# Optimization experiments

Hardware: AMD Instinct MI355X
Metric: run time of the kernel (lower is better)

## Reference

```python
import jax, jax.numpy as jnp
import numpy as np

IN_CH, OUT_CH, KS = 64, 128, 3
GRID, DEG = 8, 3
STRIDE, PAD = 1, 1
SIZE = IN_CH * KS * KS            # 576
NCOEF = GRID + DEG                # 11
GRID_RANGE = (-1.0, 1.0)


def _xavier_uniform(key, shape):
    fan_out, fan_in = shape
    a = float(np.sqrt(6.0 / (fan_in + fan_out)))
    return jax.random.uniform(key, shape, minval=-a, maxval=a, dtype=jnp.float32)


def setup_inputs() -> dict:
    key = jax.random.key(0)
    k1, k2, k3 = jax.random.split(key, 3)
    x = jax.random.normal(k1, (8, IN_CH, 32, 32), dtype=jnp.float32)
    # non-trainable knot grid, one row per unfolded feature
    knots = jnp.tile(jnp.linspace(GRID_RANGE[0], GRID_RANGE[1], GRID + 1, dtype=jnp.float32)[None, :], (SIZE, 1))
    coeff = 0.1 * jax.random.normal(k2, (OUT_CH, SIZE, NCOEF), dtype=jnp.float32)
    base_weights = _xavier_uniform(k3, (OUT_CH, SIZE))
    spline_weights = jnp.ones((OUT_CH, SIZE), dtype=jnp.float32)
    return {"x": x, "knots": knots, "coeff": coeff,
            "base_weights": base_weights, "spline_weights": spline_weights}


def bspline_basis(x, grid, k):
    # x: (S, P) evaluation points; grid: (S, G+1) knots. Returns (S, G+k, P).
    h = (grid[:, -1:] - grid[:, :1]) / (grid.shape[1] - 1)
    left = grid[:, :1] - h * jnp.arange(k, 0, -1, dtype=x.dtype)
    right = grid[:, -1:] + h * jnp.arange(1, k + 1, dtype=x.dtype)
    g = jnp.concatenate([left, grid, right], axis=1)  # (S, G+1+2k)
    xe = x[:, None, :]
    B = ((xe >= g[:, :-1, None]) & (xe < g[:, 1:, None])).astype(x.dtype)
    for d in range(1, k + 1):  # de Boor recursion over fixed degree
        B = ((xe - g[:, :-(d + 1), None]) / (g[:, d:-1, None] - g[:, :-(d + 1), None]) * B[:, :-1]
             + (g[:, d + 1:, None] - xe) / (g[:, d + 1:, None] - g[:, 1:-d, None]) * B[:, 1:])
    return B


def _unfold(x):
    # torch F.unfold with channel-major (c, kh, kw) feature ordering
    N, C, H, W = x.shape
    xp = jnp.pad(x, ((0, 0), (0, 0), (PAD, PAD), (PAD, PAD)))
    Hp = (H + 2 * PAD - KS) // STRIDE + 1
    Wp = (W + 2 * PAD - KS) // STRIDE + 1
    patches = jnp.stack([xp[:, :, i:i + STRIDE * Hp:STRIDE, j:j + STRIDE * Wp:STRIDE]
                         for i in range(KS) for j in range(KS)], axis=2)  # (N, C, KS*KS, Hp, Wp)
    L = Hp * Wp
    u = patches.reshape(N, SIZE, L)              # (N, size, L)
    u = jnp.transpose(u, (1, 0, 2)).reshape(SIZE, N * L)  # (size, N*L), col = n*L + l
    return u, Hp, Wp


def reference(x, knots, coeff, base_weights, spline_weights):
    N = x.shape[0]
    u, Hp, Wp = _unfold(x)                                   # (size, P)
    base = base_weights @ jax.nn.silu(u)                     # (Cout, P)
    B = bspline_basis(u, knots, DEG)                         # (size, ncoef, P)
    eff = spline_weights[:, :, None] * coeff                 # (Cout, size, ncoef)
    spl = jnp.einsum('csj,sjp->cp', eff, B)                  # (Cout, P)
    out = (base + spl).reshape(OUT_CH, N, Hp, Wp)
    return jnp.transpose(out, (1, 0, 2, 3))                  # (N, Cout, Hp, Wp)
```

## Files before the change

kernel.cpp:

```cpp
#include <hip/hip_runtime.h>


typedef __attribute__((ext_vector_type(8))) short bf16x8;
typedef __attribute__((ext_vector_type(4))) float f32x4;
typedef __attribute__((ext_vector_type(16))) float f32x16;
typedef __attribute__((ext_vector_type(4))) unsigned short u16x4;

#define WSWZ_BYTES 1769472
#define PHI_OFF    WSWZ_BYTES
#define PHI_BYTES  14205696
#define PART_OFF   (PHI_OFF + PHI_BYTES)

__device__ __forceinline__ short f2bf(float f) {
    union { float f; unsigned u; } c; c.f = f;
    unsigned r = c.u + 0x7fffu + ((c.u >> 16) & 1u);
    return (short)(r >> 16);
}
__device__ __forceinline__ float bf2f(unsigned short u) {
    union { unsigned u; float f; } c; c.u = ((unsigned)u) << 16;
    return c.f;
}

__global__ void kan_prep(const float* __restrict__ coeff,
                         const float* __restrict__ basew,
                         const float* __restrict__ splw,
                         const float* __restrict__ x,
                         short* __restrict__ Wswz,
                         short* __restrict__ Phi) {
    __shared__ float coeffL[6336];
    __shared__ float basewL[576];
    __shared__ float splwL[576];
    __shared__ unsigned short xs[64 * 32];
    const int t = threadIdx.x;

    if (blockIdx.x < 272) {
        const int rowid = blockIdx.x;
        const int n     = rowid / 34;
        const int ypad  = rowid - n * 34;
        const int y     = ypad - 1;
        const bool yvalid = (y >= 0 && y < 32);

        if (yvalid) {
#pragma unroll
            for (int it = 0; it < 2; ++it) {
                int cg = t + it * 256;
                int ci = cg >> 3, q = cg & 7;
                f32x4 v = *(const f32x4*)(x + (((n * 64 + ci) * 32 + y) * 32 + q * 4));
                u16x4 p;
                p.x = (unsigned short)f2bf(v.x); p.y = (unsigned short)f2bf(v.y);
                p.z = (unsigned short)f2bf(v.z); p.w = (unsigned short)f2bf(v.w);
                *(u16x4*)&xs[ci * 32 + q * 4] = p;
            }
        }
        __syncthreads();

        const size_t rowbase = (size_t)rowid * 12 * 2176;
        for (int it = t; it < 272; it += 256) {
            int xp = it >> 3, cch = it & 7, c0 = cch << 3;
            bool interior = yvalid && (xp >= 1 && xp <= 32);
            int px = xp - 1;
            int pxc = px < 0 ? 0 : (px > 31 ? 31 : px);
            bf16x8 packs[12];
#pragma unroll
            for (int j = 0; j < 8; ++j) {
                float v = interior ? bf2f(xs[(c0 + j) * 32 + pxc]) : 0.f;
                float tt = 4.f * v + 7.f;
                int   i0 = -100;
                float b0 = 0.f, b1 = 0.f, b2 = 0.f, b3 = 0.f;
                if (tt >= 0.f && tt < 14.f) {
                    i0 = (int)tt;
                    float fr  = tt - (float)i0;
                    float omf = 1.f - fr;
                    float fr2 = fr * fr, fr3 = fr2 * fr;
                    b0 = omf * omf * omf * (1.f / 6.f);
                    b1 = (3.f * fr3 - 6.f * fr2 + 4.f) * (1.f / 6.f);
                    b2 = (-3.f * fr3 + 3.f * fr2 + 3.f * fr + 1.f) * (1.f / 6.f);
                    b3 = fr3 * (1.f / 6.f);
                }
                float silu = v * __builtin_amdgcn_rcpf(1.f + __expf(-v));
                packs[0][j] = f2bf(silu);
#pragma unroll
                for (int f = 1; f < 12; ++f) {
                    int jj = f - 1;
                    float val = 0.f;
                    val = (jj == i0 - 3) ? b0 : val;
                    val = (jj == i0 - 2) ? b1 : val;
                    val = (jj == i0 - 1) ? b2 : val;
                    val = (jj == i0    ) ? b3 : val;
                    packs[f][j] = f2bf(val);
                }
            }
            int swz = (cch ^ (xp & 7)) << 3;
#pragma unroll
            for (int f = 0; f < 12; ++f)
                *(bf16x8*)&Phi[rowbase + (size_t)f * 2176 + xp * 64 + swz] = packs[f];
        }
    } else {
        const int co = blockIdx.x - 272;
        const float* crow = coeff + co * 6336;
        for (int i = t; i < 6336; i += 256) coeffL[i] = crow[i];
        for (int i = t; i < 576; i += 256) {
            basewL[i] = basew[co * 576 + i];
            splwL[i]  = splw[co * 576 + i];
        }
        __syncthreads();
        const int cb = co >> 5, lm = co & 31;
        for (int c = t; c < 864; c += 256) {
            int kk16 = c >> 1, kh = c & 1;
            int f  = kk16 / 36;
            int rm = kk16 - f * 36;
            int tap = rm >> 2, q = rm & 3;
            bf16x8 pack;
#pragma unroll
            for (int j = 0; j < 8; ++j) {
                int ci = q * 16 + kh * 8 + j;
                int s  = ci * 9 + tap;
                float v = (f == 0) ? basewL[s] : splwL[s] * coeffL[s * 11 + (f - 1)];
                pack[j] = f2bf(v);
            }
            *(bf16x8*)(Wswz + (size_t)((kk16 * 4 + cb) * 64 + kh * 32 + lm) * 8) = pack;
        }
    }
}

__global__ __launch_bounds__(256, 4)
void kan_gemm(const short* __restrict__ Phi,
              const short* __restrict__ Wswz,
              float* __restrict__ part) {
    __shared__ short Bs[2 * 8704];

    const int t  = threadIdx.x;
    const int w  = t >> 6;
    const int l  = t & 63;
    const int ln = l & 31;
    const int kh = l >> 5;

    const int fg    = blockIdx.x >> 7;
    const int ptile = blockIdx.x & 127;
    const int n     = ptile >> 4;
    const int y0    = (ptile & 15) << 1;

    const char* phiB = (const char*)Phi;
    const int planeBase = (n * 34 + y0) * 12 + fg * 2;
#pragma unroll
    for (int k = 0; k < 9; ++k) {
        int i = t + k * 256;
        if (i < 2176) {
            int pl  = i / 1088;
            int r2  = i - pl * 1088;
            int row = r2 / 272;
            int m   = r2 - row * 272;
            const char* s = phiB + (size_t)(planeBase + row * 12 + pl) * 4352 + m * 16;
            auto gsrc = (const __attribute__((address_space(1))) unsigned int*)s;
            auto ldst = (__attribute__((address_space(3))) unsigned int*)((char*)&Bs[0] + i * 16);
            __builtin_amdgcn_global_load_lds(gsrc, ldst, 16, 0, 0);
        }
    }
    __syncthreads();

    f32x16 acc[2];
#pragma unroll
    for (int pb = 0; pb < 2; ++pb)
#pragma unroll
        for (int r = 0; r < 16; ++r)
            acc[pb][r] = 0.f;

    const short* Abase = Wswz + (size_t)w * 512 + (size_t)l * 8;
#pragma unroll 1
    for (int p = 0; p < 2; ++p) {
        const short* B0 = Bs + p * 8704;
        const int kbase = (fg * 2 + p) * 36;
#pragma unroll
        for (int q = 0; q < 4; ++q) {
#pragma unroll
            for (int dx = 0; dx < 3; ++dx) {
                bf16x8 a0 = *(const bf16x8*)(Abase + (size_t)(kbase + (0 * 3 + dx) * 4 + q) * 2048);
                bf16x8 a1 = *(const bf16x8*)(Abase + (size_t)(kbase + (1 * 3 + dx) * 4 + q) * 2048);
                bf16x8 a2 = *(const bf16x8*)(Abase + (size_t)(kbase + (2 * 3 + dx) * 4 + q) * 2048);
                const int c   = q * 2 + kh;
                const int key = (ln + dx) & 7;
                bf16x8 b0, b1, b2, b3;
                {
                    int pix0 = 0 * 34 + ln + dx;
                    int pix1 = 1 * 34 + ln + dx;
                    int pix2 = 2 * 34 + ln + dx;
                    int pix3 = 3 * 34 + ln + dx;
                    int slot = (c ^ key) << 3;
                    b0 = *(const bf16x8*)&B0[pix0 * 64 + slot];
                    b1 = *(const bf16x8*)&B0[pix1 * 64 + slot];
                    b2 = *(const bf16x8*)&B0[pix2 * 64 + slot];
                    b3 = *(const bf16x8*)&B0[pix3 * 64 + slot];
                }
                acc[0] = __builtin_amdgcn_mfma_f32_32x32x16_bf16(a0, b0, acc[0], 0, 0, 0);
                acc[1] = __builtin_amdgcn_mfma_f32_32x32x16_bf16(a0, b1, acc[1], 0, 0, 0);
                acc[0] = __builtin_amdgcn_mfma_f32_32x32x16_bf16(a1, b1, acc[0], 0, 0, 0);
                acc[1] = __builtin_amdgcn_mfma_f32_32x32x16_bf16(a1, b2, acc[1], 0, 0, 0);
                acc[0] = __builtin_amdgcn_mfma_f32_32x32x16_bf16(a2, b2, acc[0], 0, 0, 0);
                acc[1] = __builtin_amdgcn_mfma_f32_32x32x16_bf16(a2, b3, acc[1], 0, 0, 0);
            }
        }
    }

    float* dst = part + (size_t)fg * 1048576;
#pragma unroll
    for (int pb = 0; pb < 2; ++pb) {
        int y = y0 + pb;
#pragma unroll
        for (int r = 0; r < 16; ++r) {
            int row = (r & 3) + 8 * (r >> 2) + 4 * kh;
            int co  = w * 32 + row;
            dst[((size_t)(n * 128 + co) * 32 + y) * 32 + ln] = acc[pb][r];
        }
    }
}

__global__ void kan_reduce(const float* __restrict__ part,
                           float* __restrict__ out) {
    const int r = blockIdx.x;
    const int p = r & 127;
    const int i = r >> 7;
    const int n  = p >> 4;
    const int yp = p & 15;
    const int c  = i * 256 + threadIdx.x;
    const int co = c >> 4;
    const int rem = c & 15;
    const int yy = rem >> 3, xq = rem & 7;
    const size_t idx = ((size_t)(n * 128 + co) * 32 + yp * 2 + yy) * 8 + xq;
    f32x4 a = ((const f32x4*)part)[idx];
#pragma unroll
    for (int s = 1; s < 6; ++s)
        a += ((const f32x4*)(part + (size_t)s * 1048576))[idx];
    ((f32x4*)out)[idx] = a;
}

extern "C" void kernel_launch(void* const* d_in, const int* in_sizes, int n_in,
                              void* d_out, int out_size, void* d_ws, size_t ws_size,
                              hipStream_t stream) {
    const float* x     = (const float*)d_in[0];
    const float* coeff = (const float*)d_in[2];
    const float* basew = (const float*)d_in[3];
    const float* splw  = (const float*)d_in[4];
    float* out = (float*)d_out;

    short* Wswz = (short*)d_ws;
    short* Phi  = (short*)((char*)d_ws + PHI_OFF);
    float* part = (float*)((char*)d_ws + PART_OFF);

    kan_prep<<<400, 256, 0, stream>>>(coeff, basew, splw, x, Wswz, Phi);
    kan_gemm<<<768, 256, 0, stream>>>(Phi, Wswz, part);
    kan_reduce<<<1024, 256, 0, stream>>>(part, out);
}
```

Measured before the change: 107.1 us.

## Fuse prep, GEMM and reduce into one cooperative kernel with grid syncs

Merges the three kernel launches into a single cooperative kernel of 768 blocks that uses grid.sync() between the prep, GEMM and reduce phases, sharing one static LDS buffer. The goal is to remove two kernel launch gaps and their tail effects. If the cooperative launch fails, it falls back to the original three launches. The cost is that the fused kernel uses the largest LDS footprint across all phases, which may reduce occupancy, and grid-wide barriers can be slow on a device with many CUs.

```diff
diff --git a/kernel.cpp b/kernel.cpp
--- a/kernel.cpp
+++ b/kernel.cpp
@@ -1,4 +1,7 @@
 #include <hip/hip_runtime.h>
+#include <hip/hip_cooperative_groups.h>
+
+namespace cg = cooperative_groups;
 
 
 typedef __attribute__((ext_vector_type(8))) short bf16x8;
@@ -21,124 +24,116 @@
     return c.f;
 }
 
-__global__ void kan_prep(const float* __restrict__ coeff,
-                         const float* __restrict__ basew,
-                         const float* __restrict__ splw,
-                         const float* __restrict__ x,
-                         short* __restrict__ Wswz,
-                         short* __restrict__ Phi) {
-    __shared__ float coeffL[6336];
-    __shared__ float basewL[576];
-    __shared__ float splwL[576];
-    __shared__ unsigned short xs[64 * 32];
-    const int t = threadIdx.x;
-
-    if (blockIdx.x < 272) {
-        const int rowid = blockIdx.x;
-        const int n     = rowid / 34;
-        const int ypad  = rowid - n * 34;
-        const int y     = ypad - 1;
-        const bool yvalid = (y >= 0 && y < 32);
-
-        if (yvalid) {
-#pragma unroll
-            for (int it = 0; it < 2; ++it) {
-                int cg = t + it * 256;
-                int ci = cg >> 3, q = cg & 7;
-                f32x4 v = *(const f32x4*)(x + (((n * 64 + ci) * 32 + y) * 32 + q * 4));
-                u16x4 p;
-                p.x = (unsigned short)f2bf(v.x); p.y = (unsigned short)f2bf(v.y);
-                p.z = (unsigned short)f2bf(v.z); p.w = (unsigned short)f2bf(v.w);
-                *(u16x4*)&xs[ci * 32 + q * 4] = p;
+
+__device__ __forceinline__ void prep_phi_body(int rowid, int t,
+                                              const float* __restrict__ x,
+                                              short* __restrict__ Phi,
+                                              unsigned short* xs ) {
+    const int n     = rowid / 34;
+    const int ypad  = rowid - n * 34;
+    const int y     = ypad - 1;
+    const bool yvalid = (y >= 0 && y < 32);
+
+    if (yvalid) {
+#pragma unroll
+        for (int it = 0; it < 2; ++it) {
+            int cg = t + it * 256;
+            int ci = cg >> 3, q = cg & 7;
+            f32x4 v = *(const f32x4*)(x + (((n * 64 + ci) * 32 + y) * 32 + q * 4));
+            u16x4 p;
+            p.x = (unsigned short)f2bf(v.x); p.y = (unsigned short)f2bf(v.y);
+            p.z = (unsigned short)f2bf(v.z); p.w = (unsigned short)f2bf(v.w);
+            *(u16x4*)&xs[ci * 32 + q * 4] = p;
+        }
+    }
+    __syncthreads();
+
+    const size_t rowbase = (size_t)rowid * 12 * 2176;
+    for (int it = t; it < 272; it += 256) {
+        int xp = it >> 3, cch = it & 7, c0 = cch << 3;
+        bool interior = yvalid && (xp >= 1 && xp <= 32);
+        int px = xp - 1;
+        int pxc = px < 0 ? 0 : (px > 31 ? 31 : px);
+        bf16x8 packs[12];
+#pragma unroll
+        for (int j = 0; j < 8; ++j) {
+            float v = interior ? bf2f(xs[(c0 + j) * 32 + pxc]) : 0.f;
+            float tt = 4.f * v + 7.f;
+            int   i0 = -100;
+            float b0 = 0.f, b1 = 0.f, b2 = 0.f, b3 = 0.f;
+            if (tt >= 0.f && tt < 14.f) {
+                i0 = (int)tt;
+                float fr  = tt - (float)i0;
+                float omf = 1.f - fr;
+                float fr2 = fr * fr, fr3 = fr2 * fr;
+                b0 = omf * omf * omf * (1.f / 6.f);
+                b1 = (3.f * fr3 - 6.f * fr2 + 4.f) * (1.f / 6.f);
+                b2 = (-3.f * fr3 + 3.f * fr2 + 3.f * fr + 1.f) * (1.f / 6.f);
+                b3 = fr3 * (1.f / 6.f);
             }
-        }
-        __syncthreads();
-
-        const size_t rowbase = (size_t)rowid * 12 * 2176;
-        for (int it = t; it < 272; it += 256) {
-            int xp = it >> 3, cch = it & 7, c0 = cch << 3;
-            bool interior = yvalid && (xp >= 1 && xp <= 32);
-            int px = xp - 1;
-            int pxc = px < 0 ? 0 : (px > 31 ? 31 : px);
-            bf16x8 packs[12];
-#pragma unroll
-            for (int j = 0; j < 8; ++j) {
-                float v = interior ? bf2f(xs[(c0 + j) * 32 + pxc]) : 0.f;
-                float tt = 4.f * v + 7.f;
-                int   i0 = -100;
-                float b0 = 0.f, b1 = 0.f, b2 = 0.f, b3 = 0.f;
-                if (tt >= 0.f && tt < 14.f) {
-                    i0 = (int)tt;
-                    float fr  = tt - (float)i0;
-                    float omf = 1.f - fr;
-                    float fr2 = fr * fr, fr3 = fr2 * fr;
-                    b0 = omf * omf * omf * (1.f / 6.f);
-                    b1 = (3.f * fr3 - 6.f * fr2 + 4.f) * (1.f / 6.f);
-                    b2 = (-3.f * fr3 + 3.f * fr2 + 3.f * fr + 1.f) * (1.f / 6.f);
-                    b3 = fr3 * (1.f / 6.f);
-                }
-                float silu = v * __builtin_amdgcn_rcpf(1.f + __expf(-v));
-                packs[0][j] = f2bf(silu);
-#pragma unroll
-                for (int f = 1; f < 12; ++f) {
-                    int jj = f - 1;
-                    float val = 0.f;
-                    val = (jj == i0 - 3) ? b0 : val;
-                    val = (jj == i0 - 2) ? b1 : val;
-                    val = (jj == i0 - 1) ? b2 : val;
-                    val = (jj == i0    ) ? b3 : val;
-                    packs[f][j] = f2bf(val);
-                }
+            float silu = v * __builtin_amdgcn_rcpf(1.f + __expf(-v));
+            packs[0][j] = f2bf(silu);
+#pragma unroll
+            for (int f = 1; f < 12; ++f) {
+                int jj = f - 1;
+                float val = 0.f;
+                val = (jj == i0 - 3) ? b0 : val;
+                val = (jj == i0 - 2) ? b1 : val;
+                val = (jj == i0 - 1) ? b2 : val;
+                val = (jj == i0    ) ? b3 : val;
+                packs[f][j] = f2bf(val);
             }
-            int swz = (cch ^ (xp & 7)) << 3;
-#pragma unroll
-            for (int f = 0; f < 12; ++f)
-                *(bf16x8*)&Phi[rowbase + (size_t)f * 2176 + xp * 64 + swz] = packs[f];
-        }
-    } else {
-        const int co = blockIdx.x - 272;
-        const float* crow = coeff + co * 6336;
-        for (int i = t; i < 6336; i += 256) coeffL[i] = crow[i];
-        for (int i = t; i < 576; i += 256) {
-            basewL[i] = basew[co * 576 + i];
-            splwL[i]  = splw[co * 576 + i];
-        }
-        __syncthreads();
-        const int cb = co >> 5, lm = co & 31;
-        for (int c = t; c < 864; c += 256) {
-            int kk16 = c >> 1, kh = c & 1;
-            int f  = kk16 / 36;
-            int rm = kk16 - f * 36;
-            int tap = rm >> 2, q = rm & 3;
-            bf16x8 pack;
-#pragma unroll
-            for (int j = 0; j < 8; ++j) {
-                int ci = q * 16 + kh * 8 + j;
-                int s  = ci * 9 + tap;
-                float v = (f == 0) ? basewL[s] : splwL[s] * coeffL[s * 11 + (f - 1)];
-                pack[j] = f2bf(v);
-            }
-            *(bf16x8*)(Wswz + (size_t)((kk16 * 4 + cb) * 64 + kh * 32 + lm) * 8) = pack;
-        }
-    }
-}
-
-__global__ __launch_bounds__(256, 4)
-void kan_gemm(const short* __restrict__ Phi,
-              const short* __restrict__ Wswz,
-              float* __restrict__ part) {
-    __shared__ short Bs[2 * 8704];
-
-    const int t  = threadIdx.x;
+        }
+        int swz = (cch ^ (xp & 7)) << 3;
+#pragma unroll
+        for (int f = 0; f < 12; ++f)
+            *(bf16x8*)&Phi[rowbase + (size_t)f * 2176 + xp * 64 + swz] = packs[f];
+    }
+}
+
+__device__ __forceinline__ void prep_w_body(int co, int t,
+                                            const float* __restrict__ coeff,
+                                            const float* __restrict__ basew,
+                                            const float* __restrict__ splw,
+                                            short* __restrict__ Wswz,
+                                            float* coeffL, float* basewL,
+                                            float* splwL) {
+    const float* crow = coeff + co * 6336;
+    for (int i = t; i < 6336; i += 256) coeffL[i] = crow[i];
+    for (int i = t; i < 576; i += 256) {
+        basewL[i] = basew[co * 576 + i];
+        splwL[i]  = splw[co * 576 + i];
+    }
+    __syncthreads();
+    const int cb = co >> 5, lm = co & 31;
+    for (int c = t; c < 864; c += 256) {
+        int kk16 = c >> 1, kh = c & 1;
+        int f  = kk16 / 36;
+        int rm = kk16 - f * 36;
+        int tap = rm >> 2, q = rm & 3;
+        bf16x8 pack;
+#pragma unroll
+        for (int j = 0; j < 8; ++j) {
+            int ci = q * 16 + kh * 8 + j;
+            int s  = ci * 9 + tap;
+            float v = (f == 0) ? basewL[s] : splwL[s] * coeffL[s * 11 + (f - 1)];
+            pack[j] = f2bf(v);
+        }
+        *(bf16x8*)(Wswz + (size_t)((kk16 * 4 + cb) * 64 + kh * 32 + lm) * 8) = pack;
+    }
+}
+
+__device__ __forceinline__ void gemm_body(int fg, int ptile, int t,
+                                          const short* __restrict__ Phi,
+                                          const short* __restrict__ Wswz,
+                                          float* __restrict__ part,
+                                          short* Bs ) {
     const int w  = t >> 6;
     const int l  = t & 63;
     const int ln = l & 31;
     const int kh = l >> 5;
-
-    const int fg    = blockIdx.x >> 7;
-    const int ptile = blockIdx.x & 127;
-    const int n     = ptile >> 4;
-    const int y0    = (ptile & 15) << 1;
+    const int n  = ptile >> 4;
+    const int y0 = (ptile & 15) << 1;
 
     const char* phiB = (const char*)Phi;
     const int planeBase = (n * 34 + y0) * 12 + fg * 2;
@@ -151,9 +146,10 @@
             int row = r2 / 272;
             int m   = r2 - row * 272;
             const char* s = phiB + (size_t)(planeBase + row * 12 + pl) * 4352 + m * 16;
-            auto gsrc = (const __attribute__((address_space(1))) unsigned int*)s;
-            auto ldst = (__attribute__((address_space(3))) unsigned int*)((char*)&Bs[0] + i * 16);
-            __builtin_amdgcn_global_load_lds(gsrc, ldst, 16, 0, 0);
+            __builtin_amdgcn_global_load_lds(
+                (const __attribute__((address_space(1))) unsigned int*)s,
+                (__attribute__((address_space(3))) unsigned int*)((char*)Bs + i * 16),
+                16, 0, 0);
         }
     }
     __syncthreads();
@@ -179,18 +175,11 @@
                 bf16x8 a2 = *(const bf16x8*)(Abase + (size_t)(kbase + (2 * 3 + dx) * 4 + q) * 2048);
                 const int c   = q * 2 + kh;
                 const int key = (ln + dx) & 7;
-                bf16x8 b0, b1, b2, b3;
-                {
-                    int pix0 = 0 * 34 + ln + dx;
-                    int pix1 = 1 * 34 + ln + dx;
-                    int pix2 = 2 * 34 + ln + dx;
-                    int pix3 = 3 * 34 + ln + dx;
-                    int slot = (c ^ key) << 3;
-                    b0 = *(const bf16x8*)&B0[pix0 * 64 + slot];
-                    b1 = *(const bf16x8*)&B0[pix1 * 64 + slot];
-                    b2 = *(const bf16x8*)&B0[pix2 * 64 + slot];
-                    b3 = *(const bf16x8*)&B0[pix3 * 64 + slot];
-                }
+                const int colb = (ln + dx) * 64 + ((c ^ key) << 3);
+                bf16x8 b0 = *(const bf16x8*)&B0[0 * 2176 + colb];
+                bf16x8 b1 = *(const bf16x8*)&B0[1 * 2176 + colb];
+                bf16x8 b2 = *(const bf16x8*)&B0[2 * 2176 + colb];
+                bf16x8 b3 = *(const bf16x8*)&B0[3 * 2176 + colb];
                 acc[0] = __builtin_amdgcn_mfma_f32_32x32x16_bf16(a0, b0, acc[0], 0, 0, 0);
                 acc[1] = __builtin_amdgcn_mfma_f32_32x32x16_bf16(a0, b1, acc[1], 0, 0, 0);
                 acc[0] = __builtin_amdgcn_mfma_f32_32x32x16_bf16(a1, b1, acc[0], 0, 0, 0);
@@ -214,14 +203,14 @@
     }
 }
 
-__global__ void kan_reduce(const float* __restrict__ part,
-                           float* __restrict__ out) {
-    const int r = blockIdx.x;
+__device__ __forceinline__ void reduce_body(int r, int t,
+                                            const float* __restrict__ part,
+                                            float* __restrict__ out) {
     const int p = r & 127;
     const int i = r >> 7;
     const int n  = p >> 4;
     const int yp = p & 15;
-    const int c  = i * 256 + threadIdx.x;
+    const int c  = i * 256 + t;
     const int co = c >> 4;
     const int rem = c & 15;
     const int yy = rem >> 3, xq = rem & 7;
@@ -231,6 +220,69 @@
     for (int s = 1; s < 6; ++s)
         a += ((const f32x4*)(part + (size_t)s * 1048576))[idx];
     ((f32x4*)out)[idx] = a;
+}
+
+__global__ __launch_bounds__(256, 4)
+void kan_fused(const float* __restrict__ coeff,
+               const float* __restrict__ basew,
+               const float* __restrict__ splw,
+               const float* __restrict__ x,
+               short* __restrict__ Wswz,
+               short* __restrict__ Phi,
+               float* __restrict__ part,
+               float* __restrict__ out) {
+    __shared__ __align__(16) char smem[34816];
+    const int t   = threadIdx.x;
+    const int bid = blockIdx.x;
+    cg::grid_group grid = cg::this_grid();
+
+    if (bid < 272) {
+        prep_phi_body(bid, t, x, Phi, (unsigned short*)smem);
+    } else if (bid < 400) {
+        float* coeffL = (float*)smem;
+        float* basewL = (float*)(smem + 25344);
+        float* splwL  = (float*)(smem + 27648);
+        prep_w_body(bid - 272, t, coeff, basew, splw, Wswz, coeffL, basewL, splwL);
+    }
+    grid.sync();
+
+    gemm_body(bid >> 7, bid & 127, t, Phi, Wswz, part, (short*)smem);
+    grid.sync();
+
+    for (int r = bid; r < 1024; r += 768)
+        reduce_body(r, t, part, out);
+}
+
+__global__ void kan_prep(const float* __restrict__ coeff,
+                         const float* __restrict__ basew,
+                         const float* __restrict__ splw,
+                         const float* __restrict__ x,
+                         short* __restrict__ Wswz,
+                         short* __restrict__ Phi) {
+    __shared__ __align__(16) char smem[34048];
+    const int t = threadIdx.x;
+    if (blockIdx.x < 272) {
+        prep_phi_body(blockIdx.x, t, x, Phi, (unsigned short*)smem);
+    } else {
+        float* coeffL = (float*)smem;
+        float* basewL = (float*)(smem + 25344);
+        float* splwL  = (float*)(smem + 27648);
+        prep_w_body(blockIdx.x - 272, t, coeff, basew, splw, Wswz,
+                    coeffL, basewL, splwL);
+    }
+}
+
+__global__ __launch_bounds__(256, 4)
+void kan_gemm(const short* __restrict__ Phi,
+              const short* __restrict__ Wswz,
+              float* __restrict__ part) {
+    __shared__ __align__(16) short Bs[2 * 8704];
+    gemm_body(blockIdx.x >> 7, blockIdx.x & 127, threadIdx.x, Phi, Wswz, part, Bs);
+}
+
+__global__ void kan_reduce(const float* __restrict__ part,
+                           float* __restrict__ out) {
+    reduce_body(blockIdx.x, threadIdx.x, part, out);
 }
 
 extern "C" void kernel_launch(void* const* d_in, const int* in_sizes, int n_in,
@@ -246,7 +298,14 @@
     short* Phi  = (short*)((char*)d_ws + PHI_OFF);
     float* part = (float*)((char*)d_ws + PART_OFF);
 
-    kan_prep<<<400, 256, 0, stream>>>(coeff, basew, splw, x, Wswz, Phi);
-    kan_gemm<<<768, 256, 0, stream>>>(Phi, Wswz, part);
-    kan_reduce<<<1024, 256, 0, stream>>>(part, out);
-}
+    void* args[] = { (void*)&coeff, (void*)&basew, (void*)&splw, (void*)&x,
+                     (void*)&Wswz, (void*)&Phi, (void*)&part, (void*)&out };
+    hipError_t e = hipLaunchCooperativeKernel((const void*)kan_fused,
+                                              dim3(768), dim3(256),
+                                              args, 0, stream);
+    if (e != hipSuccess) {
+        kan_prep<<<400, 256, 0, stream>>>(coeff, basew, splw, x, Wswz, Phi);
+        kan_gemm<<<768, 256, 0, stream>>>(Phi, Wswz, part);
+        kan_reduce<<<1024, 256, 0, stream>>>(part, out);
+    }
+}
```

After: 300.8 us. 181% more time.
